# Kernel optimization log

Measured on AMD Instinct MI355X. Metric: run time of the kernel, lower is better.

Reference implementation:

```python
import jax, jax.numpy as jnp
import numpy as np

HIDDEN = 512
HEADS = 8
D_HEAD = HIDDEN // HEADS
SCALE = D_HEAD ** -0.5
LN_EPS = 1e-5
N_L = 2048
N_R = 4096


def setup_inputs() -> dict:
    key = jax.random.key(0)
    ks = jax.random.split(key, 10)
    s = HIDDEN ** -0.5
    return {
        "q": jax.random.normal(ks[0], (N_L, HIDDEN), jnp.float32),
        "kv": jax.random.normal(ks[1], (N_R, HIDDEN), jnp.float32),
        "bias": jax.random.normal(ks[2], (N_L, N_R), jnp.float32),
        "Wq": jax.random.normal(ks[3], (HIDDEN, HIDDEN), jnp.float32) * s,
        "Wk": jax.random.normal(ks[4], (HIDDEN, HIDDEN), jnp.float32) * s,
        "Wv": jax.random.normal(ks[5], (HIDDEN, HIDDEN), jnp.float32) * s,
        "Wo": jax.random.normal(ks[6], (HIDDEN, HIDDEN), jnp.float32) * s,
        "bo": jnp.zeros((HIDDEN,), jnp.float32),
        "gamma": jnp.ones((HIDDEN,), jnp.float32),
        "beta": jnp.zeros((HIDDEN,), jnp.float32),
    }


def reference(q, kv, bias, Wq, Wk, Wv, Wo, bo, gamma, beta):
    # projections (torch Linear: x @ W.T)
    Q = (q @ Wq.T).reshape(N_L, HEADS, D_HEAD).transpose(1, 0, 2)   # [h, N_L, d]
    K = (kv @ Wk.T).reshape(N_R, HEADS, D_HEAD).transpose(1, 0, 2)  # [h, N_R, d]
    V = (kv @ Wv.T).reshape(N_R, HEADS, D_HEAD).transpose(1, 0, 2)  # [h, N_R, d]
    logits = SCALE * jnp.einsum('hld,hrd->hlr', Q, K) + bias[None]  # [h, N_L, N_R]
    attn = jax.nn.softmax(logits, axis=-1)                          # dropout p=0 -> identity
    ctx = jnp.einsum('hlr,hrd->hld', attn, V)                       # [h, N_L, d]
    ctx = ctx.transpose(1, 0, 2).reshape(N_L, HIDDEN)
    out = ctx @ Wo.T + bo
    x = out + q
    mu = jnp.mean(x, axis=-1, keepdims=True)
    var = jnp.mean((x - mu) ** 2, axis=-1, keepdims=True)
    out = (x - mu) * jax.lax.rsqrt(var + LN_EPS) * gamma + beta
    attn_mean = attn.mean(axis=0)                                   # [N_L, N_R]
    return out, attn_mean
```

## Files before the change

### kernel.cpp

```cpp
#include <hip/hip_runtime.h>
#include <hip/hip_bf16.h>
#include <stdint.h>

#define NL 2048
#define NR 4096
#define NCHUNK 8
#define CHUNK (NR / NCHUNK)
#define SCALE 0.125f
#define LN_EPS 1e-5f

typedef __attribute__((ext_vector_type(8))) short short8;
typedef __attribute__((ext_vector_type(4))) float float4v;

static __device__ __forceinline__ short f2bf(float f) {
  union { float f; uint32_t u; } v; v.f = f;
  uint32_t u = v.u;
  uint32_t r = (u + 0x7FFFu + ((u >> 16) & 1u)) >> 16;
  return (short)(r & 0xFFFFu);
}
static __device__ __forceinline__ float bf2f(short b) {
  union { uint32_t u; float f; } v; v.u = ((uint32_t)(uint16_t)b) << 16;
  return v.f;
}

__global__ void k0_cvt(const float* __restrict__ q, const float* __restrict__ kv,
                       const float* __restrict__ Wq, const float* __restrict__ Wk,
                       const float* __restrict__ Wv, const float* __restrict__ Wo,
                       short* __restrict__ qb, short* __restrict__ kvb,
                       short* __restrict__ Wqb, short* __restrict__ Wkb,
                       short* __restrict__ Wvb, short* __restrict__ Wob) {
  int i = blockIdx.x * blockDim.x + threadIdx.x;
  const float* src; short* dst;
  if (i < 131072)                 { src = q;  dst = qb;  }
  else if ((i -= 131072) < 262144){ src = kv; dst = kvb; }
  else if ((i -= 262144) < 32768) { src = Wq; dst = Wqb; }
  else if ((i -= 32768) < 32768)  { src = Wk; dst = Wkb; }
  else if ((i -= 32768) < 32768)  { src = Wv; dst = Wvb; }
  else { i -= 32768;                src = Wo; dst = Wob; }
  const float4* s4 = reinterpret_cast<const float4*>(src) + (size_t)i * 2;
  float4 a = s4[0], b = s4[1];
  short8 o;
  o[0] = f2bf(a.x); o[1] = f2bf(a.y); o[2] = f2bf(a.z); o[3] = f2bf(a.w);
  o[4] = f2bf(b.x); o[5] = f2bf(b.y); o[6] = f2bf(b.z); o[7] = f2bf(b.w);
  *reinterpret_cast<short8*>(dst + (size_t)i * 8) = o;
}

__global__ void k1_proj(const short* __restrict__ qb, const short* __restrict__ kvb,
                        const short* __restrict__ Wqb, const short* __restrict__ Wkb,
                        const short* __restrict__ Wvb,
                        short* __restrict__ Qb, short* __restrict__ Kb,
                        short* __restrict__ VT) {
  int lane = threadIdx.x & 63, warp = threadIdx.x >> 6;
  int wid = blockIdx.x * 4 + warp;
  int lr = lane & 15, lg = lane >> 4;
  const short *src, *W; short* dst; int mt, ct, mode;
  if (wid < 1024)      { src = qb;  W = Wqb; dst = Qb; mt = wid & 127; ct = wid >> 7; mode = 0; }
  else if (wid < 3072) { int id = wid - 1024; src = kvb; W = Wkb; dst = Kb; mt = id & 255; ct = id >> 8; mode = 0; }
  else                 { int id = wid - 3072; src = kvb; W = Wvb; dst = VT; mt = id & 255; ct = id >> 8; mode = 1; }
  int m0 = mt * 16, c0 = ct * 64;
  float4v acc[4] = {};
  const short* arow = src + (m0 + lr) * 512 + 8 * lg;
#pragma unroll
  for (int kk = 0; kk < 16; ++kk) {
    short8 a = *reinterpret_cast<const short8*>(arow + kk * 32);
#pragma unroll
    for (int cs = 0; cs < 4; ++cs) {
      const short* bp = W + (c0 + cs * 16 + lr) * 512 + kk * 32 + 8 * lg;
      short8 b = *reinterpret_cast<const short8*>(bp);
      acc[cs] = __builtin_amdgcn_mfma_f32_16x16x32_bf16(a, b, acc[cs], 0, 0, 0);
    }
  }
  if (mode == 0) {
#pragma unroll
    for (int cs = 0; cs < 4; ++cs)
#pragma unroll
      for (int j = 0; j < 4; ++j)
        dst[(m0 + 4 * lg + j) * 512 + c0 + cs * 16 + lr] = f2bf(acc[cs][j]);
  } else {
#pragma unroll
    for (int cs = 0; cs < 4; ++cs)
#pragma unroll
      for (int j = 0; j < 4; ++j)
        dst[(c0 + cs * 16 + lr) * 4096 + m0 + 4 * lg + j] = f2bf(acc[cs][j]);
  }
}

__global__ void __launch_bounds__(512, 8)
k2_passA(const short* __restrict__ Qb, const short* __restrict__ Kb,
         const float* __restrict__ bias, float* __restrict__ S_part) {
  int lane = threadIdx.x & 63, w = threadIdx.x >> 6;
  int lr = lane & 15, lg = lane >> 4;
  int l0 = blockIdx.x * 16;
  int chunk = blockIdx.y;
  int r_base = chunk * CHUNK;
  float sums[4] = {};
  const short* qrow = Qb + (l0 + lr) * 512 + 8 * lg;
  short8 qa0 = *reinterpret_cast<const short8*>(qrow + w * 64);
  short8 qa1 = *reinterpret_cast<const short8*>(qrow + w * 64 + 32);
#pragma unroll 1
  for (int it = 0; it < CHUNK / 32; ++it) {
    int r0 = r_base + it * 32;
    float bv[2][4];
#pragma unroll
    for (int s = 0; s < 2; ++s)
#pragma unroll
      for (int j = 0; j < 4; ++j)
        bv[s][j] = bias[(l0 + 4 * lg + j) * NR + r0 + s * 16 + lr];
    float4v cc[2];
#pragma unroll
    for (int s = 0; s < 2; ++s) {
      const short* kp = Kb + (r0 + s * 16 + lr) * 512 + w * 64 + 8 * lg;
      short8 b0 = *reinterpret_cast<const short8*>(kp);
      short8 b1 = *reinterpret_cast<const short8*>(kp + 32);
      float4v c = {};
      c = __builtin_amdgcn_mfma_f32_16x16x32_bf16(qa0, b0, c, 0, 0, 0);
      c = __builtin_amdgcn_mfma_f32_16x16x32_bf16(qa1, b1, c, 0, 0, 0);
      cc[s] = c;
    }
#pragma unroll
    for (int s = 0; s < 2; ++s)
#pragma unroll
      for (int j = 0; j < 4; ++j)
        sums[j] += __expf(SCALE * cc[s][j] + bv[s][j]);
  }
#pragma unroll
  for (int j = 0; j < 4; ++j) {
    float v = sums[j];
    v += __shfl_xor(v, 1, 64); v += __shfl_xor(v, 2, 64);
    v += __shfl_xor(v, 4, 64); v += __shfl_xor(v, 8, 64);
    sums[j] = v;
  }
  if (lr == 0) {
#pragma unroll
    for (int j = 0; j < 4; ++j)
      S_part[(chunk * 8 + w) * NL + l0 + 4 * lg + j] = sums[j];
  }
}

__global__ void k2b_reduceS(const float* __restrict__ S_part, float* __restrict__ Sinv) {
  int i = blockIdx.x * blockDim.x + threadIdx.x;
  int h = i >> 11, l = i & 2047;
  float s = 0.f;
#pragma unroll
  for (int c = 0; c < NCHUNK; ++c) s += S_part[(c * 8 + h) * NL + l];
  Sinv[i] = 1.0f / s;
}

__global__ void __launch_bounds__(512, 8)
k3_passB(const short* __restrict__ Qb, const short* __restrict__ Kb,
         const short* __restrict__ VT, const float* __restrict__ bias,
         const float* __restrict__ Sinv,
         float* __restrict__ attn_mean, short* __restrict__ ctx_part) {
  __shared__ __align__(16) short att[8][16][32];
  __shared__ float maccLDS[8][16][32];
  int lane = threadIdx.x & 63, w = threadIdx.x >> 6;
  int lr = lane & 15, lg = lane >> 4;
  int l0 = blockIdx.x * 16;
  int chunk = blockIdx.y;
  int r_base = chunk * CHUNK;
  float4v acc[4] = {};
  float sinv[4];
#pragma unroll
  for (int j = 0; j < 4; ++j)
    sinv[j] = Sinv[w * NL + l0 + 4 * lg + j];
  const short* qrow = Qb + (l0 + lr) * 512 + 8 * lg;
  short8 qa0 = *reinterpret_cast<const short8*>(qrow + w * 64);
  short8 qa1 = *reinterpret_cast<const short8*>(qrow + w * 64 + 32);
  short* myatt = &att[w][0][0];
#pragma unroll 1
  for (int it = 0; it < CHUNK / 32; ++it) {
    int r0 = r_base + it * 32;
    float bv[2][4];
#pragma unroll
    for (int s = 0; s < 2; ++s)
#pragma unroll
      for (int j = 0; j < 4; ++j)
        bv[s][j] = bias[(l0 + 4 * lg + j) * NR + r0 + s * 16 + lr];
    float4v cc[2];
#pragma unroll
    for (int s = 0; s < 2; ++s) {
      const short* kp = Kb + (r0 + s * 16 + lr) * 512 + w * 64 + 8 * lg;
      short8 b0 = *reinterpret_cast<const short8*>(kp);
      short8 b1 = *reinterpret_cast<const short8*>(kp + 32);
      float4v c = {};
      c = __builtin_amdgcn_mfma_f32_16x16x32_bf16(qa0, b0, c, 0, 0, 0);
      c = __builtin_amdgcn_mfma_f32_16x16x32_bf16(qa1, b1, c, 0, 0, 0);
      cc[s] = c;
    }
    float macc[2][4];
#pragma unroll
    for (int s = 0; s < 2; ++s)
#pragma unroll
      for (int j = 0; j < 4; ++j) {
        float e = __expf(SCALE * cc[s][j] + bv[s][j]);
        macc[s][j] = e;
        myatt[(4 * lg + j) * 32 + s * 16 + lr] = f2bf(e);
      }
    short8 pa = *reinterpret_cast<const short8*>(&att[w][lr][8 * lg]);
#pragma unroll
    for (int ds = 0; ds < 4; ++ds) {
      const short* vp = VT + (w * 64 + ds * 16 + lr) * 4096 + r0 + 8 * lg;
      short8 vb = *reinterpret_cast<const short8*>(vp);
      acc[ds] = __builtin_amdgcn_mfma_f32_16x16x32_bf16(pa, vb, acc[ds], 0, 0, 0);
    }
#pragma unroll
    for (int s = 0; s < 2; ++s)
#pragma unroll
      for (int j = 0; j < 4; ++j)
        maccLDS[w][4 * lg + j][s * 16 + lr] = macc[s][j] * sinv[j];
    __syncthreads();
    {
      int t = threadIdx.x;
      int row = t >> 5, col = t & 31;
      float v = 0.f;
#pragma unroll
      for (int hh = 0; hh < 8; ++hh) v += maccLDS[hh][row][col];
      attn_mean[(size_t)(l0 + row) * NR + r0 + col] = v * 0.125f;
    }
    __syncthreads();
  }
#pragma unroll
  for (int ds = 0; ds < 4; ++ds)
#pragma unroll
    for (int j = 0; j < 4; ++j)
      ctx_part[(chunk * NL + l0 + 4 * lg + j) * 512 + w * 64 + ds * 16 + lr] =
          f2bf(acc[ds][j] * sinv[j]);
}

__global__ void k4pre(const short* __restrict__ ctx_part, short* __restrict__ ctxsum) {
  int i = blockIdx.x * blockDim.x + threadIdx.x;
  float sm[8] = {};
#pragma unroll
  for (int c = 0; c < NCHUNK; ++c) {
    short8 v = *reinterpret_cast<const short8*>(ctx_part + (size_t)c * NL * 512 + (size_t)i * 8);
#pragma unroll
    for (int u = 0; u < 8; ++u) sm[u] += bf2f(v[u]);
  }
  short8 o;
#pragma unroll
  for (int u = 0; u < 8; ++u) o[u] = f2bf(sm[u]);
  *reinterpret_cast<short8*>(ctxsum + (size_t)i * 8) = o;
}

__global__ void k4_out(const short* __restrict__ ctxsum, const short* __restrict__ Wob,
                       const float* __restrict__ q, const float* __restrict__ bo,
                       const float* __restrict__ gamma, const float* __restrict__ beta,
                       float* __restrict__ out) {
  __shared__ float xs[16][512];
  int lane = threadIdx.x & 63, warp = threadIdx.x >> 6;
  int lr = lane & 15, lg = lane >> 4;
  int l0 = blockIdx.x * 16;
  short8 afr[16];
#pragma unroll
  for (int kk = 0; kk < 16; ++kk)
    afr[kk] = *reinterpret_cast<const short8*>(ctxsum + (l0 + lr) * 512 + kk * 32 + 8 * lg);
#pragma unroll 1
  for (int cs = 0; cs < 8; ++cs) {
    int col0 = warp * 128 + cs * 16;
    float4v c = {};
#pragma unroll
    for (int kk = 0; kk < 16; ++kk) {
      const short* bp = Wob + (col0 + lr) * 512 + kk * 32 + 8 * lg;
      short8 b = *reinterpret_cast<const short8*>(bp);
      c = __builtin_amdgcn_mfma_f32_16x16x32_bf16(afr[kk], b, c, 0, 0, 0);
    }
#pragma unroll
    for (int j = 0; j < 4; ++j) {
      int row = l0 + 4 * lg + j, col = col0 + lr;
      xs[4 * lg + j][col] = c[j] + bo[col] + q[row * 512 + col];
    }
  }
  __syncthreads();
  int tid = threadIdx.x;
  int rl = tid >> 4, g = tid & 15;
  float sum = 0.f;
#pragma unroll
  for (int i = 0; i < 32; ++i) sum += xs[rl][g + 16 * i];
  sum += __shfl_xor(sum, 1, 64); sum += __shfl_xor(sum, 2, 64);
  sum += __shfl_xor(sum, 4, 64); sum += __shfl_xor(sum, 8, 64);
  float mu = sum * (1.0f / 512.0f);
  float vs = 0.f;
#pragma unroll
  for (int i = 0; i < 32; ++i) { float d = xs[rl][g + 16 * i] - mu; vs += d * d; }
  vs += __shfl_xor(vs, 1, 64); vs += __shfl_xor(vs, 2, 64);
  vs += __shfl_xor(vs, 4, 64); vs += __shfl_xor(vs, 8, 64);
  float rs = rsqrtf(vs * (1.0f / 512.0f) + LN_EPS);
#pragma unroll
  for (int i = 0; i < 32; ++i) {
    int cc = g + 16 * i;
    out[(l0 + rl) * 512 + cc] = (xs[rl][cc] - mu) * rs * gamma[cc] + beta[cc];
  }
}

extern "C" void kernel_launch(void* const* d_in, const int* in_sizes, int n_in,
                              void* d_out, int out_size, void* d_ws, size_t ws_size,
                              hipStream_t stream) {
  const float* q     = (const float*)d_in[0];
  const float* kv    = (const float*)d_in[1];
  const float* bias  = (const float*)d_in[2];
  const float* Wq    = (const float*)d_in[3];
  const float* Wk    = (const float*)d_in[4];
  const float* Wv    = (const float*)d_in[5];
  const float* Wo    = (const float*)d_in[6];
  const float* bo    = (const float*)d_in[7];
  const float* gamma = (const float*)d_in[8];
  const float* beta  = (const float*)d_in[9];
  float* out = (float*)d_out;
  float* attn_mean = out + (size_t)NL * 512;

  char* ws = (char*)d_ws;
  short* qb       = (short*)(ws + 0);
  short* kvb      = (short*)(ws + 2097152);
  short* Wqb      = (short*)(ws + 6291456);
  short* Wkb      = (short*)(ws + 6815744);
  short* Wvb      = (short*)(ws + 7340032);
  short* Wob      = (short*)(ws + 7864320);
  short* Qb       = (short*)(ws + 8388608);
  short* Kb       = (short*)(ws + 10485760);
  short* VT       = (short*)(ws + 14680064);
  float* S_part   = (float*)(ws + 18874368);
  float* Sinv     = (float*)(ws + 19398656);
  short* ctx_part = (short*)(ws + 19464192);
  short* ctxsum   = (short*)(ws + 36241408);

  k0_cvt<<<2048, 256, 0, stream>>>(q, kv, Wq, Wk, Wv, Wo, qb, kvb, Wqb, Wkb, Wvb, Wob);
  k1_proj<<<1280, 256, 0, stream>>>(qb, kvb, Wqb, Wkb, Wvb, Qb, Kb, VT);
  k2_passA<<<dim3(128, 8), 512, 0, stream>>>(Qb, Kb, bias, S_part);
  k2b_reduceS<<<64, 256, 0, stream>>>(S_part, Sinv);
  k3_passB<<<dim3(128, 8), 512, 0, stream>>>(Qb, Kb, VT, bias, Sinv, attn_mean, ctx_part);
  k4pre<<<512, 256, 0, stream>>>(ctx_part, ctxsum);
  k4_out<<<128, 256, 0, stream>>>(ctxsum, Wob, q, bo, gamma, beta, out);
}
```

Baseline: 374.0 us.

## Pipeline bias loads and restructure attention pass B around LDS-staged bias and probabilities

Pass A now software-pipelines the bias loads across two register buffers, so the next iteration's bias reads overlap the current MFMA and exp work. Pass B stages bias tiles through a double-buffered, coalesced LDS buffer. It swaps the MFMA operand order so each lane computes a transposed score fragment, folds the 1/sum normalization into the probabilities, and writes them with packed bf16 conversion. The head-averaged attention output is now read from the shared bf16 probability tile, which removes the separate fp32 staging buffer and one barrier per iteration. In exchange, attn_mean is accumulated from bf16-rounded values, which lowers its precision.

Measured after the change: 373.8 us. Within noise of the previous version (-0.1%).

```diff
diff --git a/kernel.cpp b/kernel.cpp
--- a/kernel.cpp
+++ b/kernel.cpp
@@ -21,6 +21,11 @@
 static __device__ __forceinline__ float bf2f(short b) {
   union { uint32_t u; float f; } v; v.u = ((uint32_t)(uint16_t)b) << 16;
   return v.f;
+}
+static __device__ __forceinline__ uint32_t cvtpk(float a, float b) {
+  uint32_t r;
+  asm("v_cvt_pk_bf16_f32 %0, %1, %2" : "=v"(r) : "v"(a), "v"(b));
+  return r;
 }
 
 __global__ void k0_cvt(const float* __restrict__ q, const float* __restrict__ kv,
@@ -85,6 +90,30 @@
   }
 }
 
+#define K2_LOADB(dst, itv)                                                    \
+  {                                                                           \
+    int r0n = r_base + (itv) * 32;                                            \
+    _Pragma("unroll") for (int s = 0; s < 2; ++s)                             \
+    _Pragma("unroll") for (int j = 0; j < 4; ++j)                             \
+      dst[s][j] = bias[(l0 + 4 * lg + j) * (size_t)NR + r0n + s * 16 + lr];   \
+  }
+#define K2_BODY(bv, itv)                                                      \
+  {                                                                           \
+    int r0 = r_base + (itv) * 32;                                             \
+    float4v cc[2];                                                            \
+    _Pragma("unroll") for (int s = 0; s < 2; ++s) {                           \
+      const short* kp = Kb + (r0 + s * 16 + lr) * 512 + w * 64 + 8 * lg;      \
+      short8 b0 = *reinterpret_cast<const short8*>(kp);                       \
+      short8 b1 = *reinterpret_cast<const short8*>(kp + 32);                  \
+      float4v c = {};                                                         \
+      c = __builtin_amdgcn_mfma_f32_16x16x32_bf16(qa0, b0, c, 0, 0, 0);       \
+      c = __builtin_amdgcn_mfma_f32_16x16x32_bf16(qa1, b1, c, 0, 0, 0);       \
+      cc[s] = c;                                                              \
+    }                                                                         \
+    _Pragma("unroll") for (int s = 0; s < 2; ++s)                             \
+    _Pragma("unroll") for (int j = 0; j < 4; ++j)                             \
+      sums[j] += __expf(fmaf(SCALE, cc[s][j], bv[s][j]));                     \
+  }
 __global__ void __launch_bounds__(512, 8)
 k2_passA(const short* __restrict__ Qb, const short* __restrict__ Kb,
          const float* __restrict__ bias, float* __restrict__ S_part) {
@@ -97,134 +126,101 @@
   const short* qrow = Qb + (l0 + lr) * 512 + 8 * lg;
   short8 qa0 = *reinterpret_cast<const short8*>(qrow + w * 64);
   short8 qa1 = *reinterpret_cast<const short8*>(qrow + w * 64 + 32);
+  float bvA[2][4], bvB[2][4];
+  K2_LOADB(bvA, 0)
+#pragma unroll 1
+  for (int it2 = 0; it2 < 8; ++it2) {
+    K2_LOADB(bvB, 2 * it2 + 1)
+    K2_BODY(bvA, 2 * it2)
+    if (it2 < 7) K2_LOADB(bvA, 2 * it2 + 2)
+    K2_BODY(bvB, 2 * it2 + 1)
+  }
+#pragma unroll
+  for (int j = 0; j < 4; ++j) {
+    float v = sums[j];
+    v += __shfl_xor(v, 1, 64); v += __shfl_xor(v, 2, 64);
+    v += __shfl_xor(v, 4, 64); v += __shfl_xor(v, 8, 64);
+    sums[j] = v;
+  }
+  if (lr == 0) {
+#pragma unroll
+    for (int j = 0; j < 4; ++j)
+      S_part[(chunk * 8 + w) * NL + l0 + 4 * lg + j] = sums[j];
+  }
+}
+
+__global__ void k2b_reduceS(const float* __restrict__ S_part, float* __restrict__ Sinv) {
+  int i = blockIdx.x * blockDim.x + threadIdx.x;
+  int h = i >> 11, l = i & 2047;
+  float s = 0.f;
+#pragma unroll
+  for (int c = 0; c < NCHUNK; ++c) s += S_part[(c * 8 + h) * NL + l];
+  Sinv[i] = 1.0f / s;
+}
+
+__global__ void __launch_bounds__(512, 8)
+k3_passB(const short* __restrict__ Qb, const short* __restrict__ Kb,
+         const short* __restrict__ VT, const float* __restrict__ bias,
+         const float* __restrict__ Sinv,
+         float* __restrict__ attn_mean, short* __restrict__ ctx_part) {
+  __shared__ __align__(16) short P[8][2][16][40];
+  __shared__ float BIAS[2][16][33];
+  int t = threadIdx.x;
+  int lane = t & 63, w = t >> 6;
+  int lr = lane & 15, lg = lane >> 4;
+  int l0 = blockIdx.x * 16;
+  int chunk = blockIdx.y;
+  int r_base = chunk * CHUNK;
+  float4v acc[4] = {};
+  float sinv = Sinv[w * NL + l0 + lr];
+  const short* qrow = Qb + (l0 + lr) * 512 + 8 * lg;
+  short8 qa0 = *reinterpret_cast<const short8*>(qrow + w * 64);
+  short8 qa1 = *reinterpret_cast<const short8*>(qrow + w * 64 + 32);
+  int sq = t >> 5, sr = t & 31;
+  BIAS[0][sq][sr] = bias[(l0 + sq) * (size_t)NR + r_base + sr];
+  __syncthreads();
 #pragma unroll 1
   for (int it = 0; it < CHUNK / 32; ++it) {
+    int cb = it & 1;
     int r0 = r_base + it * 32;
-    float bv[2][4];
-#pragma unroll
-    for (int s = 0; s < 2; ++s)
-#pragma unroll
-      for (int j = 0; j < 4; ++j)
-        bv[s][j] = bias[(l0 + 4 * lg + j) * NR + r0 + s * 16 + lr];
-    float4v cc[2];
+    if (it < CHUNK / 32 - 1)
+      BIAS[cb ^ 1][sq][sr] = bias[(l0 + sq) * (size_t)NR + r0 + 32 + sr];
 #pragma unroll
     for (int s = 0; s < 2; ++s) {
       const short* kp = Kb + (r0 + s * 16 + lr) * 512 + w * 64 + 8 * lg;
       short8 b0 = *reinterpret_cast<const short8*>(kp);
       short8 b1 = *reinterpret_cast<const short8*>(kp + 32);
       float4v c = {};
-      c = __builtin_amdgcn_mfma_f32_16x16x32_bf16(qa0, b0, c, 0, 0, 0);
-      c = __builtin_amdgcn_mfma_f32_16x16x32_bf16(qa1, b1, c, 0, 0, 0);
-      cc[s] = c;
-    }
-#pragma unroll
-    for (int s = 0; s < 2; ++s)
-#pragma unroll
-      for (int j = 0; j < 4; ++j)
-        sums[j] += __expf(SCALE * cc[s][j] + bv[s][j]);
-  }
-#pragma unroll
-  for (int j = 0; j < 4; ++j) {
-    float v = sums[j];
-    v += __shfl_xor(v, 1, 64); v += __shfl_xor(v, 2, 64);
-    v += __shfl_xor(v, 4, 64); v += __shfl_xor(v, 8, 64);
-    sums[j] = v;
-  }
-  if (lr == 0) {
-#pragma unroll
-    for (int j = 0; j < 4; ++j)
-      S_part[(chunk * 8 + w) * NL + l0 + 4 * lg + j] = sums[j];
-  }
-}
-
-__global__ void k2b_reduceS(const float* __restrict__ S_part, float* __restrict__ Sinv) {
-  int i = blockIdx.x * blockDim.x + threadIdx.x;
-  int h = i >> 11, l = i & 2047;
-  float s = 0.f;
-#pragma unroll
-  for (int c = 0; c < NCHUNK; ++c) s += S_part[(c * 8 + h) * NL + l];
-  Sinv[i] = 1.0f / s;
-}
-
-__global__ void __launch_bounds__(512, 8)
-k3_passB(const short* __restrict__ Qb, const short* __restrict__ Kb,
-         const short* __restrict__ VT, const float* __restrict__ bias,
-         const float* __restrict__ Sinv,
-         float* __restrict__ attn_mean, short* __restrict__ ctx_part) {
-  __shared__ __align__(16) short att[8][16][32];
-  __shared__ float maccLDS[8][16][32];
-  int lane = threadIdx.x & 63, w = threadIdx.x >> 6;
-  int lr = lane & 15, lg = lane >> 4;
-  int l0 = blockIdx.x * 16;
-  int chunk = blockIdx.y;
-  int r_base = chunk * CHUNK;
-  float4v acc[4] = {};
-  float sinv[4];
-#pragma unroll
-  for (int j = 0; j < 4; ++j)
-    sinv[j] = Sinv[w * NL + l0 + 4 * lg + j];
-  const short* qrow = Qb + (l0 + lr) * 512 + 8 * lg;
-  short8 qa0 = *reinterpret_cast<const short8*>(qrow + w * 64);
-  short8 qa1 = *reinterpret_cast<const short8*>(qrow + w * 64 + 32);
-  short* myatt = &att[w][0][0];
-#pragma unroll 1
-  for (int it = 0; it < CHUNK / 32; ++it) {
-    int r0 = r_base + it * 32;
-    float bv[2][4];
-#pragma unroll
-    for (int s = 0; s < 2; ++s)
-#pragma unroll
-      for (int j = 0; j < 4; ++j)
-        bv[s][j] = bias[(l0 + 4 * lg + j) * NR + r0 + s * 16 + lr];
-    float4v cc[2];
-#pragma unroll
-    for (int s = 0; s < 2; ++s) {
-      const short* kp = Kb + (r0 + s * 16 + lr) * 512 + w * 64 + 8 * lg;
-      short8 b0 = *reinterpret_cast<const short8*>(kp);
-      short8 b1 = *reinterpret_cast<const short8*>(kp + 32);
-      float4v c = {};
-      c = __builtin_amdgcn_mfma_f32_16x16x32_bf16(qa0, b0, c, 0, 0, 0);
-      c = __builtin_amdgcn_mfma_f32_16x16x32_bf16(qa1, b1, c, 0, 0, 0);
-      cc[s] = c;
-    }
-    float macc[2][4];
-#pragma unroll
-    for (int s = 0; s < 2; ++s)
-#pragma unroll
-      for (int j = 0; j < 4; ++j) {
-        float e = __expf(SCALE * cc[s][j] + bv[s][j]);
-        macc[s][j] = e;
-        myatt[(4 * lg + j) * 32 + s * 16 + lr] = f2bf(e);
-      }
-    short8 pa = *reinterpret_cast<const short8*>(&att[w][lr][8 * lg]);
+      c = __builtin_amdgcn_mfma_f32_16x16x32_bf16(b0, qa0, c, 0, 0, 0);
+      c = __builtin_amdgcn_mfma_f32_16x16x32_bf16(b1, qa1, c, 0, 0, 0);
+      float e0 = __expf(fmaf(SCALE, c[0], BIAS[cb][lr][s * 16 + 4 * lg + 0])) * sinv;
+      float e1 = __expf(fmaf(SCALE, c[1], BIAS[cb][lr][s * 16 + 4 * lg + 1])) * sinv;
+      float e2 = __expf(fmaf(SCALE, c[2], BIAS[cb][lr][s * 16 + 4 * lg + 2])) * sinv;
+      float e3 = __expf(fmaf(SCALE, c[3], BIAS[cb][lr][s * 16 + 4 * lg + 3])) * sinv;
+      uint2 pk; pk.x = cvtpk(e0, e1); pk.y = cvtpk(e2, e3);
+      *reinterpret_cast<uint2*>(&P[w][cb][lr][s * 16 + 4 * lg]) = pk;
+    }
+    short8 pa = *reinterpret_cast<const short8*>(&P[w][cb][lr][8 * lg]);
 #pragma unroll
     for (int ds = 0; ds < 4; ++ds) {
       const short* vp = VT + (w * 64 + ds * 16 + lr) * 4096 + r0 + 8 * lg;
       short8 vb = *reinterpret_cast<const short8*>(vp);
       acc[ds] = __builtin_amdgcn_mfma_f32_16x16x32_bf16(pa, vb, acc[ds], 0, 0, 0);
     }
-#pragma unroll
-    for (int s = 0; s < 2; ++s)
-#pragma unroll
-      for (int j = 0; j < 4; ++j)
-        maccLDS[w][4 * lg + j][s * 16 + lr] = macc[s][j] * sinv[j];
     __syncthreads();
     {
-      int t = threadIdx.x;
-      int row = t >> 5, col = t & 31;
       float v = 0.f;
 #pragma unroll
-      for (int hh = 0; hh < 8; ++hh) v += maccLDS[hh][row][col];
-      attn_mean[(size_t)(l0 + row) * NR + r0 + col] = v * 0.125f;
-    }
-    __syncthreads();
+      for (int hh = 0; hh < 8; ++hh) v += bf2f(P[hh][cb][sq][sr]);
+      attn_mean[(size_t)(l0 + sq) * NR + r0 + sr] = v * 0.125f;
+    }
   }
 #pragma unroll
   for (int ds = 0; ds < 4; ++ds)
 #pragma unroll
     for (int j = 0; j < 4; ++j)
       ctx_part[(chunk * NL + l0 + 4 * lg + j) * 512 + w * 64 + ds * 16 + lr] =
-          f2bf(acc[ds][j] * sinv[j]);
+          f2bf(acc[ds][j]);
 }
 
 __global__ void k4pre(const short* __restrict__ ctx_part, short* __restrict__ ctxsum) {
```
